# Kernel tuning notes

Measured on AMD Instinct MI355X. Metric: run time of the kernel, lower is better.

The kernel has to match this reference:

```python
import jax, jax.numpy as jnp
import numpy as np

N, E, P = 10000, 160000, 4000
ND, ED, H, C = 8, 3, 4, 64     # node_dim, edge_dim, heads, hidden_dim (=out channels/head)
D1 = H * C                     # 256, concat output of each GATv2 layer


def setup_inputs():
    key = jax.random.key(0)
    ks = jax.random.split(key, 40)
    g = lambda k, shp, s=0.05: (jax.random.normal(k, shp, jnp.float32) * s)
    x = jax.random.normal(ks[0], (N, ND), jnp.float32)
    src = jax.random.randint(ks[1], (E,), 0, N)
    dst = jax.random.randint(ks[2], (E,), 0, N)
    edge_index = jnp.stack([src, dst])                     # [2,E]
    edge_attr = jax.random.normal(ks[3], (E, ED), jnp.float32)
    physical_edges = edge_index[:, :P].T                   # [P,2], guaranteed hits
    inp = dict(x=x, edge_index=edge_index, edge_attr=edge_attr, physical_edges=physical_edges)
    # GATv2 layer 1: in ND -> H*C (lin_l, lin_r with bias; lin_edge no bias; att [H,C]; final bias)
    inp.update(Wl1=g(ks[4], (ND, H * C)), bl1=g(ks[5], (H * C,)),
               Wr1=g(ks[6], (ND, H * C)), br1=g(ks[7], (H * C,)),
               We1=g(ks[8], (ED, H * C)), att1=g(ks[9], (H, C)), b1=g(ks[10], (H * C,)))
    # GATv2 layer 2: in D1 -> H*C
    inp.update(Wl2=g(ks[11], (D1, H * C)), bl2=g(ks[12], (H * C,)),
               Wr2=g(ks[13], (D1, H * C)), br2=g(ks[14], (H * C,)),
               We2=g(ks[15], (ED, H * C)), att2=g(ks[16], (H, C)), b2=g(ks[17], (H * C,)))
    # edge_q_net: Linear(2*D1+ED -> C), Linear(C -> C//2), Linear(C//2 -> 1)
    inp.update(Wq1=g(ks[18], (2 * D1 + ED, C)), bq1=g(ks[19], (C,)),
               Wq2=g(ks[20], (C, C // 2)), bq2=g(ks[21], (C // 2,)),
               Wq3=g(ks[22], (C // 2, 1)), bq3=g(ks[23], (1,)))
    # node_q_net: Linear(D1 -> C), Linear(C -> C//2), Linear(C//2 -> 1)
    inp.update(Wn1=g(ks[24], (D1, C)), bn1=g(ks[25], (C,)),
               Wn2=g(ks[26], (C, C // 2)), bn2=g(ks[27], (C // 2,)),
               Wn3=g(ks[28], (C // 2, 1)), bn3=g(ks[29], (1,)))
    return inp


def gatv2(x, src, dst, e_attr, Wl, bl, Wr, br, We, att, bias):
    """PyG GATv2Conv with edge_dim, concat=True. Returns [N, H*C]."""
    xl = (x @ Wl + bl).reshape(-1, H, C)          # source transform  [N,H,C]
    xr = (x @ Wr + br).reshape(-1, H, C)          # target transform  [N,H,C]
    ee = (e_attr @ We).reshape(-1, H, C)          # edge transform    [E,H,C]
    m = jax.nn.leaky_relu(xl[src] + xr[dst] + ee, 0.2)   # [E,H,C]
    logits = jnp.einsum('ehc,hc->eh', m, att)            # [E,H]
    amax = jax.ops.segment_max(logits, dst, num_segments=N)
    ex = jnp.exp(logits - amax[dst])
    den = jax.ops.segment_sum(ex, dst, num_segments=N) + 1e-16
    alpha = ex / den[dst]                                 # softmax over incoming edges
    out = jax.ops.segment_sum(alpha[:, :, None] * xl[src], dst, num_segments=N)
    return out.reshape(-1, H * C) + bias


def reference(x, edge_index, edge_attr, physical_edges,
              Wl1, bl1, Wr1, br1, We1, att1, b1,
              Wl2, bl2, Wr2, br2, We2, att2, b2,
              Wq1, bq1, Wq2, bq2, Wq3, bq3,
              Wn1, bn1, Wn2, bn2, Wn3, bn3):
    src, dst = edge_index[0], edge_index[1]
    h = jax.nn.elu(gatv2(x, src, dst, edge_attr, Wl1, bl1, Wr1, br1, We1, att1, b1))
    h = jax.nn.elu(gatv2(h, src, dst, edge_attr, Wl2, bl2, Wr2, br2, We2, att2, b2))

    # vectorized replacement of the per-physical-edge Python loop:
    # first matching edge index for (i,j) or (j,i); zeros if absent.
    keys = src * N + dst                           # unique key per directed edge (fits int32)
    order = jnp.argsort(keys)                      # stable -> smallest original index first
    skeys = keys[order]
    i, j = physical_edges[:, 0], physical_edges[:, 1]

    def first_idx(q):
        pos = jnp.clip(jnp.searchsorted(skeys, q), 0, E - 1)
        fnd = skeys[pos] == q
        return jnp.where(fnd, order[pos], E), fnd   # E = sentinel (> any valid idx)

    i1, f1 = first_idx(i * N + j)
    i2, f2 = first_idx(j * N + i)
    idx = jnp.minimum(i1, i2)                       # first index of combined mask
    found = f1 | f2
    efeat = jnp.where(found[:, None], edge_attr[jnp.clip(idx, 0, E - 1)], 0.0)   # [P,ED]

    ef = jnp.concatenate([h[i], h[j], efeat], axis=-1)                # [P, 2*D1+ED]
    eq = jax.nn.elu(ef @ Wq1 + bq1)
    eq = jax.nn.elu(eq @ Wq2 + bq2)
    entangle_q = (eq @ Wq3 + bq3)[:, 0]                               # [P]

    nq = jax.nn.elu(h @ Wn1 + bn1)
    nq = jax.nn.elu(nq @ Wn2 + bn2)
    swap_q = (nq @ Wn3 + bn3)[:, 0]                                   # [N]
    return entangle_q, swap_q
```

## Files before the change

kernel.cpp:

```cpp
#include <hip/hip_runtime.h>
#include <cmath>

constexpr int kN  = 10000;
constexpr int kE  = 160000;
constexpr int kP  = 4000;
constexpr int kND = 8;
constexpr int kH  = 4;
constexpr int kC  = 64;
constexpr int kD1 = kH * kC;
constexpr int kEFS  = 2 * kD1 + 3;
constexpr int kEFSP = 544;

constexpr unsigned kTblSize = 1u << 19;
constexpr unsigned kTblMask = kTblSize - 1;
constexpr unsigned kEmpty   = 0xFFFFFFFFu;

typedef __attribute__((ext_vector_type(8))) short bf16x8;
typedef __attribute__((ext_vector_type(4))) float f32x4;

__device__ __forceinline__ unsigned short f2bf(float f) {
  unsigned u = __float_as_uint(f);
  unsigned r = (u + 0x7FFFu + ((u >> 16) & 1u)) >> 16;
  return (unsigned short)r;
}
__device__ __forceinline__ float bf2f(unsigned short u) {
  return __uint_as_float(((unsigned)u) << 16);
}

__device__ __forceinline__ unsigned hash_u32(unsigned k) {
  k *= 2654435761u;
  k ^= k >> 16;
  return k & kTblMask;
}

constexpr int kGemmBX    = (kN + 63) / 64;
constexpr int kGemmBlk   = kGemmBX * 8;
constexpr int kHistBlk   = (kE + 255) / 256;
constexpr int kCvtElems  = 2 * 256 * 256 + 64 * kEFSP + 64 * 256;
constexpr int kCvtBlk    = (kCvtElems + 255) / 256;
constexpr int kMegaBlk   = kGemmBlk + kHistBlk + kCvtBlk;

__launch_bounds__(256)
__global__ void mega1_k(const float* __restrict__ x,
                        const float* __restrict__ Wl1, const float* __restrict__ bl1,
                        const float* __restrict__ Wr1, const float* __restrict__ br1,
                        unsigned short* __restrict__ xl_bf, unsigned short* __restrict__ xr_bf,
                        const int* __restrict__ src, const int* __restrict__ dst,
                        int* __restrict__ counts, unsigned* __restrict__ tbl,
                        const float* __restrict__ Wl2, const float* __restrict__ Wr2,
                        const float* __restrict__ Wq1, const float* __restrict__ Wn1,
                        unsigned short* __restrict__ Wl2t, unsigned short* __restrict__ Wr2t,
                        unsigned short* __restrict__ Wq1t, unsigned short* __restrict__ Wn1t) {
  __shared__ __align__(16) float s_a[8][68];
  __shared__ __align__(16) float s_w[8][64];
  int bi = blockIdx.x;
  int tid = threadIdx.x;
  if (bi < kGemmBlk) {
    int bx = bi % kGemmBX, by = bi / kGemmBX;
    int r0 = bx * 64;
    const float* W; const float* bb; unsigned short* outp;
    if (by < 4) { W = Wl1; bb = bl1; outp = xl_bf; }
    else        { W = Wr1; bb = br1; outp = xr_bf; by -= 4; }
    int cbase = by * 64;
#pragma unroll
    for (int f = tid; f < 512; f += 256) {
      int rr = f >> 3, kk = f & 7;
      int r = r0 + rr;
      s_a[kk][rr] = (r < kN) ? x[(size_t)r * kND + kk] : 0.f;
    }
#pragma unroll
    for (int f = tid; f < 512; f += 256) {
      int kk = f >> 6, cc = f & 63;
      s_w[kk][cc] = W[(size_t)kk * kD1 + cbase + cc];
    }
    __syncthreads();
    int tx = tid & 15, ty = tid >> 4;
    float acc[4][4];
#pragma unroll
    for (int i = 0; i < 4; i++)
#pragma unroll
      for (int j = 0; j < 4; j++) acc[i][j] = 0.f;
#pragma unroll
    for (int kk = 0; kk < 8; kk++) {
      float4 av = *(const float4*)&s_a[kk][ty * 4];
      float4 wv = *(const float4*)&s_w[kk][tx * 4];
      float a4[4] = {av.x, av.y, av.z, av.w};
      float w4[4] = {wv.x, wv.y, wv.z, wv.w};
#pragma unroll
      for (int i = 0; i < 4; i++)
#pragma unroll
        for (int j = 0; j < 4; j++) acc[i][j] = fmaf(a4[i], w4[j], acc[i][j]);
    }
    int c = cbase + tx * 4;
    float b4[4] = {bb[c], bb[c + 1], bb[c + 2], bb[c + 3]};
#pragma unroll
    for (int i = 0; i < 4; i++) {
      int r = r0 + ty * 4 + i;
      if (r < kN) {
        ushort4 v;
        v.x = f2bf(acc[i][0] + b4[0]); v.y = f2bf(acc[i][1] + b4[1]);
        v.z = f2bf(acc[i][2] + b4[2]); v.w = f2bf(acc[i][3] + b4[3]);
        *(ushort4*)&outp[(size_t)r * kD1 + c] = v;
      }
    }
  } else if (bi < kGemmBlk + kHistBlk) {
    int e = (bi - kGemmBlk) * 256 + tid;
    if (e >= kE) return;
    int d = dst[e];
    atomicAdd(&counts[d], 1);
    unsigned key = (unsigned)src[e] * (unsigned)kN + (unsigned)d;
    unsigned h = hash_u32(key);
    for (;;) {
      unsigned prev = atomicCAS(&tbl[2 * h], kEmpty, key);
      if (prev == kEmpty || prev == key) {
        atomicMin(&tbl[2 * h + 1], (unsigned)e);
        return;
      }
      h = (h + 1) & kTblMask;
    }
  } else {
    const int s0 = 256 * 256, s1 = 2 * s0, s2 = s1 + 64 * kEFSP, s3 = s2 + 64 * 256;
    int idx = (bi - kGemmBlk - kHistBlk) * 256 + tid;
    if (idx < s0) {
      int n = idx >> 8, k = idx & 255;
      Wl2t[idx] = f2bf(Wl2[(size_t)k * 256 + n]);
    } else if (idx < s1) {
      int q = idx - s0;
      int n = q >> 8, k = q & 255;
      Wr2t[q] = f2bf(Wr2[(size_t)k * 256 + n]);
    } else if (idx < s2) {
      int q = idx - s1;
      int n = q / kEFSP, k = q - n * kEFSP;
      Wq1t[q] = (k < kEFS) ? f2bf(Wq1[(size_t)k * 64 + n]) : (unsigned short)0;
    } else if (idx < s3) {
      int q = idx - s2;
      int n = q >> 8, k = q & 255;
      Wn1t[q] = f2bf(Wn1[(size_t)k * 64 + n]);
    }
  }
}

__launch_bounds__(1024)
__global__ void scan_k(const int* __restrict__ counts, int* __restrict__ row_ptr,
                       int* __restrict__ cursor) {
  __shared__ int wsum[16];
  int tid = threadIdx.x;
  int lane = tid & 63, w = tid >> 6;
  int base = tid * 10;
  int v[10];
  int tot = 0;
#pragma unroll
  for (int i = 0; i < 10; i++) {
    int idx = base + i;
    v[i] = (idx < kN) ? (counts[idx] + 1) : 0;
    tot += v[i];
  }
  int inc = tot;
#pragma unroll
  for (int o = 1; o < 64; o <<= 1) {
    int t = __shfl_up(inc, o);
    if (lane >= o) inc += t;
  }
  if (lane == 63) wsum[w] = inc;
  __syncthreads();
  int woff = 0;
  for (int q = 0; q < w; q++) woff += wsum[q];
  int run = woff + inc - tot;
#pragma unroll
  for (int i = 0; i < 10; i++) {
    int idx = base + i;
    if (idx < kN) { row_ptr[idx] = run; cursor[idx] = run; }
    run += v[i];
  }
  if (tid == 0) row_ptr[kN] = kE;
}

__global__ void scatter_k(const int* __restrict__ src, const int* __restrict__ dst,
                          const float* __restrict__ edge_attr,
                          int* __restrict__ cursor, float4* __restrict__ rec) {
  int e = blockIdx.x * blockDim.x + threadIdx.x;
  if (e >= kE) return;
  int d = dst[e];
  int pos = atomicAdd(&cursor[d], 1);
  float4 r;
  r.x = __int_as_float(src[e]);
  r.y = edge_attr[e * 3 + 0];
  r.z = edge_attr[e * 3 + 1];
  r.w = edge_attr[e * 3 + 2];
  rec[pos] = r;
}

template <int ACT>
__launch_bounds__(256)
__global__ void mgemm_k(const unsigned short* __restrict__ in, int M, int Kp,
                        const unsigned short* __restrict__ Wt0,
                        const float* __restrict__ b0, unsigned short* __restrict__ out0,
                        const unsigned short* __restrict__ Wt1,
                        const float* __restrict__ b1, unsigned short* __restrict__ out1,
                        int N, int nby) {
  __shared__ __align__(16) short s_a[64][32];
  __shared__ __align__(16) short s_b[64][32];
  int tid = threadIdx.x;
  int l = tid & 63, w = tid >> 6;
  int r0 = blockIdx.x * 64;
  int by = blockIdx.y;
  const unsigned short* Wt = Wt0; const float* bb = b0; unsigned short* outv = out0;
  if (by >= nby) { Wt = Wt1; bb = b1; outv = out1; by -= nby; }
  int cbase = by * 64;

  int sr = tid >> 2;
  int skc = tid & 3;

  f32x4 acc[4];
#pragma unroll
  for (int c = 0; c < 4; c++) acc[c] = (f32x4){0.f, 0.f, 0.f, 0.f};

  int m_frag = l & 15, quad = l >> 4;

  for (int k0 = 0; k0 < Kp; k0 += 32) {
    bf16x8 av = {0, 0, 0, 0, 0, 0, 0, 0};
    int r = r0 + sr;
    if (r < M) av = *(const bf16x8*)&in[(size_t)r * Kp + k0 + skc * 8];
    *(bf16x8*)&s_a[sr][skc * 8] = av;
    bf16x8 bv = *(const bf16x8*)&Wt[(size_t)(cbase + sr) * Kp + k0 + skc * 8];
    *(bf16x8*)&s_b[sr][skc * 8] = bv;
    __syncthreads();
    bf16x8 af = *(const bf16x8*)&s_a[w * 16 + m_frag][quad * 8];
#pragma unroll
    for (int c = 0; c < 4; c++) {
      bf16x8 bfr = *(const bf16x8*)&s_b[c * 16 + m_frag][quad * 8];
      acc[c] = __builtin_amdgcn_mfma_f32_16x16x32_bf16(af, bfr, acc[c], 0, 0, 0);
    }
    __syncthreads();
  }

#pragma unroll
  for (int c = 0; c < 4; c++) {
    int col = cbase + c * 16 + m_frag;
    float bv = bb[col];
#pragma unroll
    for (int i = 0; i < 4; i++) {
      int r = r0 + w * 16 + quad * 4 + i;
      if (r < M) {
        float u = acc[c][i] + bv;
        if (ACT == 1) u = (u > 0.f) ? u : expm1f(u);
        outv[(size_t)r * N + col] = f2bf(u);
      }
    }
  }
}

__launch_bounds__(256)
__global__ void gat_k(const unsigned short* __restrict__ xl_bf,
                      const unsigned short* __restrict__ xr_bf,
                      const int* __restrict__ row_ptr, const float4* __restrict__ rec,
                      const float* __restrict__ We, const float* __restrict__ att,
                      const float* __restrict__ bias, unsigned short* __restrict__ out_bf) {
  __shared__ float sA[4][4][64];
  __shared__ float sS[4][64];
  int n = blockIdx.x;
  int tid = threadIdx.x;
  int l = tid & 63, w = tid >> 6;
  int c0 = (l >> 4) * kC + (l & 15) * 4;

  ushort4 xrv = *(const ushort4*)&xr_bf[(size_t)n * kD1 + c0];
  float4 xr_c = {bf2f(xrv.x), bf2f(xrv.y), bf2f(xrv.z), bf2f(xrv.w)};
  float4 we0 = *(const float4*)&We[0 * kD1 + c0];
  float4 we1 = *(const float4*)&We[1 * kD1 + c0];
  float4 we2 = *(const float4*)&We[2 * kD1 + c0];
  float4 at4 = *(const float4*)&att[c0];

  int row = row_ptr[n], end = row_ptr[n + 1];
  float S = 0.f;
  float A0 = 0.f, A1 = 0.f, A2 = 0.f, A3 = 0.f;

  int k = row + w;
  float4 rA, rB; ushort4 xA, xB;
  if (k < end) {
    rA = rec[k];
    xA = *(const ushort4*)&xl_bf[(size_t)__float_as_int(rA.x) * kD1 + c0];
  }
  if (k + 4 < end) {
    rB = rec[k + 4];
    xB = *(const ushort4*)&xl_bf[(size_t)__float_as_int(rB.x) * kD1 + c0];
  }
  for (; k < end; k += 4) {
    float4 rc = rA; ushort4 xc = xA;
    rA = rB; xA = xB;
    if (k + 8 < end) {
      rB = rec[k + 8];
      xB = *(const ushort4*)&xl_bf[(size_t)__float_as_int(rB.x) * kD1 + c0];
    }
    float x0 = bf2f(xc.x), x1 = bf2f(xc.y), x2 = bf2f(xc.z), x3 = bf2f(xc.w);
    float m0 = x0 + xr_c.x + fmaf(rc.y, we0.x, fmaf(rc.z, we1.x, rc.w * we2.x));
    float m1 = x1 + xr_c.y + fmaf(rc.y, we0.y, fmaf(rc.z, we1.y, rc.w * we2.y));
    float m2 = x2 + xr_c.z + fmaf(rc.y, we0.z, fmaf(rc.z, we1.z, rc.w * we2.z));
    float m3 = x3 + xr_c.w + fmaf(rc.y, we0.w, fmaf(rc.z, we1.w, rc.w * we2.w));
    m0 = fmaxf(m0, 0.2f * m0); m1 = fmaxf(m1, 0.2f * m1);
    m2 = fmaxf(m2, 0.2f * m2); m3 = fmaxf(m3, 0.2f * m3);
    float t = fmaf(m0, at4.x, fmaf(m1, at4.y, fmaf(m2, at4.z, m3 * at4.w)));
    t += __shfl_xor(t, 1);
    t += __shfl_xor(t, 2);
    t += __shfl_xor(t, 4);
    t += __shfl_xor(t, 8);
    float wgt = __expf(t);
    S += wgt;
    A0 = fmaf(wgt, x0, A0); A1 = fmaf(wgt, x1, A1);
    A2 = fmaf(wgt, x2, A2); A3 = fmaf(wgt, x3, A3);
  }
  sA[w][0][l] = A0; sA[w][1][l] = A1; sA[w][2][l] = A2; sA[w][3][l] = A3;
  sS[w][l] = S;
  __syncthreads();
  if (w == 0) {
    float St = sS[0][l] + sS[1][l] + sS[2][l] + sS[3][l];
    float T0 = sA[0][0][l] + sA[1][0][l] + sA[2][0][l] + sA[3][0][l];
    float T1 = sA[0][1][l] + sA[1][1][l] + sA[2][1][l] + sA[3][1][l];
    float T2 = sA[0][2][l] + sA[1][2][l] + sA[2][2][l] + sA[3][2][l];
    float T3 = sA[0][3][l] + sA[1][3][l] + sA[2][3][l] + sA[3][3][l];
    float inv = 1.f / (St + 1e-16f);
    float4 b4 = *(const float4*)&bias[c0];
    float u0 = fmaf(T0, inv, b4.x), u1 = fmaf(T1, inv, b4.y);
    float u2 = fmaf(T2, inv, b4.z), u3 = fmaf(T3, inv, b4.w);
    u0 = (u0 > 0.f) ? u0 : expm1f(u0);
    u1 = (u1 > 0.f) ? u1 : expm1f(u1);
    u2 = (u2 > 0.f) ? u2 : expm1f(u2);
    u3 = (u3 > 0.f) ? u3 : expm1f(u3);
    ushort4 ov;
    ov.x = f2bf(u0); ov.y = f2bf(u1); ov.z = f2bf(u2); ov.w = f2bf(u3);
    *(ushort4*)&out_bf[(size_t)n * kD1 + c0] = ov;
  }
}

constexpr int kEheadBlk = (kP + 63) / 64;
constexpr int kNheadBlk = (kN + 63) / 64;

__launch_bounds__(256)
__global__ void heads_k(const unsigned short* __restrict__ h_bf, const int* __restrict__ pe,
                        const float* __restrict__ edge_attr, const unsigned* __restrict__ tbl,
                        const unsigned short* __restrict__ Wqt, const float* __restrict__ bq1,
                        const float* __restrict__ Wq2, const float* __restrict__ bq2,
                        const float* __restrict__ Wq3, const float* __restrict__ bq3,
                        const unsigned short* __restrict__ Wnt, const float* __restrict__ bn1,
                        const float* __restrict__ Wn2, const float* __restrict__ bn2,
                        const float* __restrict__ Wn3, const float* __restrict__ bn3,
                        float* __restrict__ out_e, float* __restrict__ out_n) {
  __shared__ union {
    struct { short a[64][32]; short b[64][32]; } st;
    float u[64][65];
  } sm;
  __shared__ int s_i[64], s_j[64];
  __shared__ unsigned short s_ea[64][4];
  int tid = threadIdx.x;
  int l = tid & 63, w = tid >> 6;
  int sr = tid >> 2, skc = tid & 3;
  int m_frag = l & 15, quad = l >> 4;

  f32x4 acc[4];
#pragma unroll
  for (int c = 0; c < 4; c++) acc[c] = (f32x4){0.f, 0.f, 0.f, 0.f};

  if (blockIdx.x < kEheadBlk) {
    int r0 = blockIdx.x * 64;
    if (tid < 64) {
      int p = r0 + tid;
      int i = 0, j = 0;
      unsigned short e0 = 0, e1 = 0, e2 = 0;
      if (p < kP) {
        i = pe[p * 2 + 0]; j = pe[p * 2 + 1];
        unsigned best = kEmpty;
        unsigned keys[2] = { (unsigned)i * (unsigned)kN + (unsigned)j,
                             (unsigned)j * (unsigned)kN + (unsigned)i };
        for (int q = 0; q < 2; q++) {
          unsigned key = keys[q];
          unsigned hsh = hash_u32(key);
          for (;;) {
            unsigned k2 = tbl[2 * hsh];
            if (k2 == kEmpty) break;
            if (k2 == key) {
              unsigned v = tbl[2 * hsh + 1];
              if (v < best) best = v;
              break;
            }
            hsh = (hsh + 1) & kTblMask;
          }
        }
        if (best != kEmpty) {
          e0 = f2bf(edge_attr[best * 3 + 0]);
          e1 = f2bf(edge_attr[best * 3 + 1]);
          e2 = f2bf(edge_attr[best * 3 + 2]);
        }
      }
      s_i[tid] = i; s_j[tid] = j;
      s_ea[tid][0] = e0; s_ea[tid][1] = e1; s_ea[tid][2] = e2; s_ea[tid][3] = 0;
    }
    __syncthreads();

    for (int k0 = 0; k0 < kEFSP; k0 += 32) {
      int gk = k0 + skc * 8;
      bf16x8 av;
      if (gk < 256) {
        av = *(const bf16x8*)&h_bf[(size_t)s_i[sr] * kD1 + gk];
      } else if (gk < 512) {
        av = *(const bf16x8*)&h_bf[(size_t)s_j[sr] * kD1 + (gk - 256)];
      } else {
        av = (bf16x8){0, 0, 0, 0, 0, 0, 0, 0};
        if (gk == 512) {
          av[0] = (short)s_ea[sr][0];
          av[1] = (short)s_ea[sr][1];
          av[2] = (short)s_ea[sr][2];
        }
      }
      *(bf16x8*)&sm.st.a[sr][skc * 8] = av;
      bf16x8 bv = *(const bf16x8*)&Wqt[(size_t)sr * kEFSP + k0 + skc * 8];
      *(bf16x8*)&sm.st.b[sr][skc * 8] = bv;
      __syncthreads();
      bf16x8 af = *(const bf16x8*)&sm.st.a[w * 16 + m_frag][quad * 8];
#pragma unroll
      for (int c = 0; c < 4; c++) {
        bf16x8 bfr = *(const bf16x8*)&sm.st.b[c * 16 + m_frag][quad * 8];
        acc[c] = __builtin_amdgcn_mfma_f32_16x16x32_bf16(af, bfr, acc[c], 0, 0, 0);
      }
      __syncthreads();
    }

#pragma unroll
    for (int c = 0; c < 4; c++) {
      int col = c * 16 + m_frag;
      float bv = bq1[col];
#pragma unroll
      for (int i = 0; i < 4; i++) {
        float u = acc[c][i] + bv;
        u = (u > 0.f) ? u : expm1f(u);
        sm.u[w * 16 + quad * 4 + i][col] = u;
      }
    }
    __syncthreads();

    int c2 = tid & 31, rb = (tid >> 5) * 8;
    float a2[8];
#pragma unroll
    for (int i = 0; i < 8; i++) a2[i] = 0.f;
    for (int k = 0; k < 64; k++) {
      float wv = Wq2[k * 32 + c2];
#pragma unroll
      for (int i = 0; i < 8; i++) a2[i] = fmaf(sm.u[rb + i][k], wv, a2[i]);
    }
    float w3 = Wq3[c2], bb2 = bq2[c2], bb3 = bq3[0];
#pragma unroll
    for (int i = 0; i < 8; i++) {
      float u = a2[i] + bb2;
      u = (u > 0.f) ? u : expm1f(u);
      float p = u * w3;
      p += __shfl_xor(p, 1);
      p += __shfl_xor(p, 2);
      p += __shfl_xor(p, 4);
      p += __shfl_xor(p, 8);
      p += __shfl_xor(p, 16);
      int r = r0 + rb + i;
      if (c2 == 0 && r < kP) out_e[r] = p + bb3;
    }
  } else {
    int r0 = (blockIdx.x - kEheadBlk) * 64;
    for (int k0 = 0; k0 < kD1; k0 += 32) {
      bf16x8 av = {0, 0, 0, 0, 0, 0, 0, 0};
      int r = r0 + sr;
      if (r < kN) av = *(const bf16x8*)&h_bf[(size_t)r * kD1 + k0 + skc * 8];
      *(bf16x8*)&sm.st.a[sr][skc * 8] = av;
      bf16x8 bv = *(const bf16x8*)&Wnt[(size_t)sr * kD1 + k0 + skc * 8];
      *(bf16x8*)&sm.st.b[sr][skc * 8] = bv;
      __syncthreads();
      bf16x8 af = *(const bf16x8*)&sm.st.a[w * 16 + m_frag][quad * 8];
#pragma unroll
      for (int c = 0; c < 4; c++) {
        bf16x8 bfr = *(const bf16x8*)&sm.st.b[c * 16 + m_frag][quad * 8];
        acc[c] = __builtin_amdgcn_mfma_f32_16x16x32_bf16(af, bfr, acc[c], 0, 0, 0);
      }
      __syncthreads();
    }

#pragma unroll
    for (int c = 0; c < 4; c++) {
      int col = c * 16 + m_frag;
      float bv = bn1[col];
#pragma unroll
      for (int i = 0; i < 4; i++) {
        float u = acc[c][i] + bv;
        u = (u > 0.f) ? u : expm1f(u);
        sm.u[w * 16 + quad * 4 + i][col] = u;
      }
    }
    __syncthreads();

    int c2 = tid & 31, rb = (tid >> 5) * 8;
    float a2[8];
#pragma unroll
    for (int i = 0; i < 8; i++) a2[i] = 0.f;
    for (int k = 0; k < 64; k++) {
      float wv = Wn2[k * 32 + c2];
#pragma unroll
      for (int i = 0; i < 8; i++) a2[i] = fmaf(sm.u[rb + i][k], wv, a2[i]);
    }
    float w3 = Wn3[c2], bb2 = bn2[c2], bb3 = bn3[0];
#pragma unroll
    for (int i = 0; i < 8; i++) {
      float u = a2[i] + bb2;
      u = (u > 0.f) ? u : expm1f(u);
      float p = u * w3;
      p += __shfl_xor(p, 1);
      p += __shfl_xor(p, 2);
      p += __shfl_xor(p, 4);
      p += __shfl_xor(p, 8);
      p += __shfl_xor(p, 16);
      int r = r0 + rb + i;
      if (c2 == 0 && r < kN) out_n[r] = p + bb3;
    }
  }
}

extern "C" void kernel_launch(void* const* d_in, const int* in_sizes, int n_in,
                              void* d_out, int out_size, void* d_ws, size_t ws_size,
                              hipStream_t stream) {
  const float* x          = (const float*)d_in[0];
  const int*   edge_index = (const int*)d_in[1];
  const float* edge_attr  = (const float*)d_in[2];
  const int*   pe         = (const int*)d_in[3];
  const float* Wl1 = (const float*)d_in[4];
  const float* bl1 = (const float*)d_in[5];
  const float* Wr1 = (const float*)d_in[6];
  const float* br1 = (const float*)d_in[7];
  const float* We1 = (const float*)d_in[8];
  const float* att1= (const float*)d_in[9];
  const float* b1  = (const float*)d_in[10];
  const float* Wl2 = (const float*)d_in[11];
  const float* bl2 = (const float*)d_in[12];
  const float* Wr2 = (const float*)d_in[13];
  const float* br2 = (const float*)d_in[14];
  const float* We2 = (const float*)d_in[15];
  const float* att2= (const float*)d_in[16];
  const float* b2  = (const float*)d_in[17];
  const float* Wq1 = (const float*)d_in[18];
  const float* bq1 = (const float*)d_in[19];
  const float* Wq2 = (const float*)d_in[20];
  const float* bq2 = (const float*)d_in[21];
  const float* Wq3 = (const float*)d_in[22];
  const float* bq3 = (const float*)d_in[23];
  const float* Wn1 = (const float*)d_in[24];
  const float* bn1 = (const float*)d_in[25];
  const float* Wn2 = (const float*)d_in[26];
  const float* bn2 = (const float*)d_in[27];
  const float* Wn3 = (const float*)d_in[28];
  const float* bn3 = (const float*)d_in[29];

  const int* src = edge_index;
  const int* dst = edge_index + kE;

  char* ws = (char*)d_ws;
  size_t off = 0;
  auto alloc = [&](size_t bytes) -> char* {
    char* p = ws + off;
    off += (bytes + 255) & ~(size_t)255;
    return p;
  };
  unsigned short* xl_bf = (unsigned short*)alloc((size_t)kN * kD1 * 2);
  unsigned short* xr_bf = (unsigned short*)alloc((size_t)kN * kD1 * 2);
  unsigned short* h_bf  = (unsigned short*)alloc((size_t)kN * kD1 * 2);
  unsigned short* Wl2t  = (unsigned short*)alloc((size_t)kD1 * kD1 * 2);
  unsigned short* Wr2t  = (unsigned short*)alloc((size_t)kD1 * kD1 * 2);
  unsigned short* Wq1t  = (unsigned short*)alloc((size_t)64 * kEFSP * 2);
  unsigned short* Wn1t  = (unsigned short*)alloc((size_t)64 * kD1 * 2);
  int* row_ptr    = (int*)alloc((kN + 1) * 4);
  int* cursor     = (int*)alloc(kN * 4);
  float4* rec     = (float4*)alloc((size_t)kE * 16);
  int* counts     = (int*)alloc(kN * 4);
  unsigned* tbl   = (unsigned*)alloc((size_t)kTblSize * 2 * 4);
  size_t initBytes = ((char*)tbl - (char*)counts) + (size_t)kTblSize * 2 * 4;

  hipMemsetAsync(counts, 0xFF, initBytes, stream);

  mega1_k<<<kMegaBlk, 256, 0, stream>>>(x, Wl1, bl1, Wr1, br1, xl_bf, xr_bf,
                                        src, dst, counts, tbl,
                                        Wl2, Wr2, Wq1, Wn1,
                                        Wl2t, Wr2t, Wq1t, Wn1t);
  scan_k<<<1, 1024, 0, stream>>>(counts, row_ptr, cursor);
  scatter_k<<<(kE + 255) / 256, 256, 0, stream>>>(src, dst, edge_attr, cursor, rec);

  gat_k<<<kN, 256, 0, stream>>>(xl_bf, xr_bf, row_ptr, rec, We1, att1, b1, h_bf);
  mgemm_k<0><<<dim3(kGemmBX, 8), 256, 0, stream>>>(h_bf, kN, kD1,
                                                   Wl2t, bl2, xl_bf,
                                                   Wr2t, br2, xr_bf, kD1, 4);
  gat_k<<<kN, 256, 0, stream>>>(xl_bf, xr_bf, row_ptr, rec, We2, att2, b2, h_bf);

  heads_k<<<kEheadBlk + kNheadBlk, 256, 0, stream>>>(h_bf, pe, edge_attr, tbl,
                                                     Wq1t, bq1, Wq2, bq2, Wq3, bq3,
                                                     Wn1t, bn1, Wn2, bn2, Wn3, bn3,
                                                     (float*)d_out, (float*)d_out + kP);
}
```

Measured before the change: 263.8 us.

## Fuse layer-1 linear projections into GAT aggregation kernel, recomputing from raw features

Removes the layer-1 xl/xr GEMM from the setup megakernel. A new gat1_k recomputes x@Wl1+bl1 per edge from the 8-dim source features, and x@Wr1+br1 per destination node, directly in registers. This avoids writing and re-reading the two bf16 [N,256] intermediates. In exchange each edge does 32 extra FMAs per lane, and layer-1 values stay in fp32 rather than being rounded to bf16.

After: 296.5 us. 12.4% more time.

```diff
diff --git a/kernel.cpp b/kernel.cpp
--- a/kernel.cpp
+++ b/kernel.cpp
@@ -34,77 +34,22 @@
 }
 
 constexpr int kGemmBX    = (kN + 63) / 64;
-constexpr int kGemmBlk   = kGemmBX * 8;
 constexpr int kHistBlk   = (kE + 255) / 256;
 constexpr int kCvtElems  = 2 * 256 * 256 + 64 * kEFSP + 64 * 256;
 constexpr int kCvtBlk    = (kCvtElems + 255) / 256;
-constexpr int kMegaBlk   = kGemmBlk + kHistBlk + kCvtBlk;
+constexpr int kMegaBlk   = kHistBlk + kCvtBlk;
 
 __launch_bounds__(256)
-__global__ void mega1_k(const float* __restrict__ x,
-                        const float* __restrict__ Wl1, const float* __restrict__ bl1,
-                        const float* __restrict__ Wr1, const float* __restrict__ br1,
-                        unsigned short* __restrict__ xl_bf, unsigned short* __restrict__ xr_bf,
-                        const int* __restrict__ src, const int* __restrict__ dst,
+__global__ void mega1_k(const int* __restrict__ src, const int* __restrict__ dst,
                         int* __restrict__ counts, unsigned* __restrict__ tbl,
                         const float* __restrict__ Wl2, const float* __restrict__ Wr2,
                         const float* __restrict__ Wq1, const float* __restrict__ Wn1,
                         unsigned short* __restrict__ Wl2t, unsigned short* __restrict__ Wr2t,
                         unsigned short* __restrict__ Wq1t, unsigned short* __restrict__ Wn1t) {
-  __shared__ __align__(16) float s_a[8][68];
-  __shared__ __align__(16) float s_w[8][64];
   int bi = blockIdx.x;
   int tid = threadIdx.x;
-  if (bi < kGemmBlk) {
-    int bx = bi % kGemmBX, by = bi / kGemmBX;
-    int r0 = bx * 64;
-    const float* W; const float* bb; unsigned short* outp;
-    if (by < 4) { W = Wl1; bb = bl1; outp = xl_bf; }
-    else        { W = Wr1; bb = br1; outp = xr_bf; by -= 4; }
-    int cbase = by * 64;
-#pragma unroll
-    for (int f = tid; f < 512; f += 256) {
-      int rr = f >> 3, kk = f & 7;
-      int r = r0 + rr;
-      s_a[kk][rr] = (r < kN) ? x[(size_t)r * kND + kk] : 0.f;
-    }
-#pragma unroll
-    for (int f = tid; f < 512; f += 256) {
-      int kk = f >> 6, cc = f & 63;
-      s_w[kk][cc] = W[(size_t)kk * kD1 + cbase + cc];
-    }
-    __syncthreads();
-    int tx = tid & 15, ty = tid >> 4;
-    float acc[4][4];
-#pragma unroll
-    for (int i = 0; i < 4; i++)
-#pragma unroll
-      for (int j = 0; j < 4; j++) acc[i][j] = 0.f;
-#pragma unroll
-    for (int kk = 0; kk < 8; kk++) {
-      float4 av = *(const float4*)&s_a[kk][ty * 4];
-      float4 wv = *(const float4*)&s_w[kk][tx * 4];
-      float a4[4] = {av.x, av.y, av.z, av.w};
-      float w4[4] = {wv.x, wv.y, wv.z, wv.w};
-#pragma unroll
-      for (int i = 0; i < 4; i++)
-#pragma unroll
-        for (int j = 0; j < 4; j++) acc[i][j] = fmaf(a4[i], w4[j], acc[i][j]);
-    }
-    int c = cbase + tx * 4;
-    float b4[4] = {bb[c], bb[c + 1], bb[c + 2], bb[c + 3]};
-#pragma unroll
-    for (int i = 0; i < 4; i++) {
-      int r = r0 + ty * 4 + i;
-      if (r < kN) {
-        ushort4 v;
-        v.x = f2bf(acc[i][0] + b4[0]); v.y = f2bf(acc[i][1] + b4[1]);
-        v.z = f2bf(acc[i][2] + b4[2]); v.w = f2bf(acc[i][3] + b4[3]);
-        *(ushort4*)&outp[(size_t)r * kD1 + c] = v;
-      }
-    }
-  } else if (bi < kGemmBlk + kHistBlk) {
-    int e = (bi - kGemmBlk) * 256 + tid;
+  if (bi < kHistBlk) {
+    int e = bi * 256 + tid;
     if (e >= kE) return;
     int d = dst[e];
     atomicAdd(&counts[d], 1);
@@ -120,7 +65,7 @@
     }
   } else {
     const int s0 = 256 * 256, s1 = 2 * s0, s2 = s1 + 64 * kEFSP, s3 = s2 + 64 * 256;
-    int idx = (bi - kGemmBlk - kHistBlk) * 256 + tid;
+    int idx = (bi - kHistBlk) * 256 + tid;
     if (idx < s0) {
       int n = idx >> 8, k = idx & 255;
       Wl2t[idx] = f2bf(Wl2[(size_t)k * 256 + n]);
@@ -247,6 +192,118 @@
         outv[(size_t)r * N + col] = f2bf(u);
       }
     }
+  }
+}
+
+__launch_bounds__(256)
+__global__ void gat1_k(const float* __restrict__ x,
+                       const float* __restrict__ Wl1, const float* __restrict__ bl1,
+                       const float* __restrict__ Wr1, const float* __restrict__ br1,
+                       const int* __restrict__ row_ptr, const float4* __restrict__ rec,
+                       const float* __restrict__ We, const float* __restrict__ att,
+                       const float* __restrict__ bias, unsigned short* __restrict__ out_bf) {
+  __shared__ float sA[4][4][64];
+  __shared__ float sS[4][64];
+  int n = blockIdx.x;
+  int tid = threadIdx.x;
+  int l = tid & 63, w = tid >> 6;
+  int c0 = (l >> 4) * kC + (l & 15) * 4;
+
+  float4 wl[8];
+#pragma unroll
+  for (int kk = 0; kk < 8; kk++) wl[kk] = *(const float4*)&Wl1[kk * kD1 + c0];
+  float4 blv = *(const float4*)&bl1[c0];
+
+  float4 we0 = *(const float4*)&We[0 * kD1 + c0];
+  float4 we1 = *(const float4*)&We[1 * kD1 + c0];
+  float4 we2 = *(const float4*)&We[2 * kD1 + c0];
+  float4 at4 = *(const float4*)&att[c0];
+
+  float4 xn0 = *(const float4*)&x[(size_t)n * kND];
+  float4 xn1 = *(const float4*)&x[(size_t)n * kND + 4];
+  float xnk[8] = {xn0.x, xn0.y, xn0.z, xn0.w, xn1.x, xn1.y, xn1.z, xn1.w};
+  float4 xr_c = *(const float4*)&br1[c0];
+#pragma unroll
+  for (int kk = 0; kk < 8; kk++) {
+    float4 wr = *(const float4*)&Wr1[kk * kD1 + c0];
+    xr_c.x = fmaf(xnk[kk], wr.x, xr_c.x);
+    xr_c.y = fmaf(xnk[kk], wr.y, xr_c.y);
+    xr_c.z = fmaf(xnk[kk], wr.z, xr_c.z);
+    xr_c.w = fmaf(xnk[kk], wr.w, xr_c.w);
+  }
+
+  int row = row_ptr[n], end = row_ptr[n + 1];
+  float S = 0.f;
+  float A0 = 0.f, A1 = 0.f, A2 = 0.f, A3 = 0.f;
+
+  int k = row + w;
+  float4 rA, rB, aA0, aA1, aB0, aB1;
+  if (k < end) {
+    rA = rec[k];
+    int s = __float_as_int(rA.x);
+    aA0 = *(const float4*)&x[(size_t)s * kND];
+    aA1 = *(const float4*)&x[(size_t)s * kND + 4];
+  }
+  if (k + 4 < end) {
+    rB = rec[k + 4];
+    int s = __float_as_int(rB.x);
+    aB0 = *(const float4*)&x[(size_t)s * kND];
+    aB1 = *(const float4*)&x[(size_t)s * kND + 4];
+  }
+  for (; k < end; k += 4) {
+    float4 rc = rA; float4 a0 = aA0, a1 = aA1;
+    rA = rB; aA0 = aB0; aA1 = aB1;
+    if (k + 8 < end) {
+      rB = rec[k + 8];
+      int s = __float_as_int(rB.x);
+      aB0 = *(const float4*)&x[(size_t)s * kND];
+      aB1 = *(const float4*)&x[(size_t)s * kND + 4];
+    }
+    float xk[8] = {a0.x, a0.y, a0.z, a0.w, a1.x, a1.y, a1.z, a1.w};
+    float x0 = blv.x, x1 = blv.y, x2 = blv.z, x3 = blv.w;
+#pragma unroll
+    for (int kk = 0; kk < 8; kk++) {
+      x0 = fmaf(xk[kk], wl[kk].x, x0);
+      x1 = fmaf(xk[kk], wl[kk].y, x1);
+      x2 = fmaf(xk[kk], wl[kk].z, x2);
+      x3 = fmaf(xk[kk], wl[kk].w, x3);
+    }
+    float m0 = x0 + xr_c.x + fmaf(rc.y, we0.x, fmaf(rc.z, we1.x, rc.w * we2.x));
+    float m1 = x1 + xr_c.y + fmaf(rc.y, we0.y, fmaf(rc.z, we1.y, rc.w * we2.y));
+    float m2 = x2 + xr_c.z + fmaf(rc.y, we0.z, fmaf(rc.z, we1.z, rc.w * we2.z));
+    float m3 = x3 + xr_c.w + fmaf(rc.y, we0.w, fmaf(rc.z, we1.w, rc.w * we2.w));
+    m0 = fmaxf(m0, 0.2f * m0); m1 = fmaxf(m1, 0.2f * m1);
+    m2 = fmaxf(m2, 0.2f * m2); m3 = fmaxf(m3, 0.2f * m3);
+    float t = fmaf(m0, at4.x, fmaf(m1, at4.y, fmaf(m2, at4.z, m3 * at4.w)));
+    t += __shfl_xor(t, 1);
+    t += __shfl_xor(t, 2);
+    t += __shfl_xor(t, 4);
+    t += __shfl_xor(t, 8);
+    float wgt = __expf(t);
+    S += wgt;
+    A0 = fmaf(wgt, x0, A0); A1 = fmaf(wgt, x1, A1);
+    A2 = fmaf(wgt, x2, A2); A3 = fmaf(wgt, x3, A3);
+  }
+  sA[w][0][l] = A0; sA[w][1][l] = A1; sA[w][2][l] = A2; sA[w][3][l] = A3;
+  sS[w][l] = S;
+  __syncthreads();
+  if (w == 0) {
+    float St = sS[0][l] + sS[1][l] + sS[2][l] + sS[3][l];
+    float T0 = sA[0][0][l] + sA[1][0][l] + sA[2][0][l] + sA[3][0][l];
+    float T1 = sA[0][1][l] + sA[1][1][l] + sA[2][1][l] + sA[3][1][l];
+    float T2 = sA[0][2][l] + sA[1][2][l] + sA[2][2][l] + sA[3][2][l];
+    float T3 = sA[0][3][l] + sA[1][3][l] + sA[2][3][l] + sA[3][3][l];
+    float inv = 1.f / (St + 1e-16f);
+    float4 b4 = *(const float4*)&bias[c0];
+    float u0 = fmaf(T0, inv, b4.x), u1 = fmaf(T1, inv, b4.y);
+    float u2 = fmaf(T2, inv, b4.z), u3 = fmaf(T3, inv, b4.w);
+    u0 = (u0 > 0.f) ? u0 : expm1f(u0);
+    u1 = (u1 > 0.f) ? u1 : expm1f(u1);
+    u2 = (u2 > 0.f) ? u2 : expm1f(u2);
+    u3 = (u3 > 0.f) ? u3 : expm1f(u3);
+    ushort4 ov;
+    ov.x = f2bf(u0); ov.y = f2bf(u1); ov.z = f2bf(u2); ov.w = f2bf(u3);
+    *(ushort4*)&out_bf[(size_t)n * kD1 + c0] = ov;
   }
 }
 
@@ -577,14 +634,14 @@
 
   hipMemsetAsync(counts, 0xFF, initBytes, stream);
 
-  mega1_k<<<kMegaBlk, 256, 0, stream>>>(x, Wl1, bl1, Wr1, br1, xl_bf, xr_bf,
-                                        src, dst, counts, tbl,
+  mega1_k<<<kMegaBlk, 256, 0, stream>>>(src, dst, counts, tbl,
                                         Wl2, Wr2, Wq1, Wn1,
                                         Wl2t, Wr2t, Wq1t, Wn1t);
   scan_k<<<1, 1024, 0, stream>>>(counts, row_ptr, cursor);
   scatter_k<<<(kE + 255) / 256, 256, 0, stream>>>(src, dst, edge_attr, cursor, rec);
 
-  gat_k<<<kN, 256, 0, stream>>>(xl_bf, xr_bf, row_ptr, rec, We1, att1, b1, h_bf);
+  gat1_k<<<kN, 256, 0, stream>>>(x, Wl1, bl1, Wr1, br1, row_ptr, rec,
+                                 We1, att1, b1, h_bf);
   mgemm_k<0><<<dim3(kGemmBX, 8), 256, 0, stream>>>(h_bf, kN, kD1,
                                                    Wl2t, bl2, xl_bf,
                                                    Wr2t, br2, xr_bf, kD1, 4);
```
